# Kernel tuning notes

Hardware: AMD Instinct MI355X
Metric: run time of the kernel (lower is better)

Reference implementation:

```python
import jax, jax.numpy as jnp
import numpy as np
import math

# dims matching init_kwargs
B, N, CS, CZ = 1, 512, 384, 128
H, C, PQ, PV = 8, 128, 8, 8
INF, EPS = 1e5, 1e-8

# ---- quaternion / motor helpers (PGA motor encoded as [qw,qx,qy,qz,tx,ty,tz,0]) ----

def quat_conj(q):
    return q * jnp.array([1.0, -1.0, -1.0, -1.0], q.dtype)

def quat_mul(a, b):
    aw, ax, ay, az = jnp.split(a, 4, -1)
    bw, bx, by, bz = jnp.split(b, 4, -1)
    return jnp.concatenate([
        aw*bw - ax*bx - ay*by - az*bz,
        aw*bx + ax*bw + ay*bz - az*by,
        aw*by - ax*bz + ay*bw + az*bx,
        aw*bz + ax*by - ay*bx + az*bw], -1)

def quat_rotate(q, v):
    qv = q[..., 1:]
    uv = jnp.cross(qv, v)
    uuv = jnp.cross(qv, uv)
    return v + 2.0 * (q[..., :1] * uv + uuv)

def point_trafo(p, q, t):
    # p [...,K,3]; rigid transform by frame motor, homogeneous 4-vector out
    pp = quat_rotate(q, p) + t
    return jnp.concatenate([pp, jnp.ones_like(pp[..., :1])], -1)

def mv_transform(mv, q, t):
    # versor sandwich on a 16-dim multivector: three rotatable 3-vector blocks,
    # the point block (7:10, weight at 10) also translates; slots 0 and 10:16 invariant
    s0 = mv[..., 0:1]
    v1 = quat_rotate(q, mv[..., 1:4])
    v2 = quat_rotate(q, mv[..., 4:7])
    w = mv[..., 10:11]
    p = quat_rotate(q, mv[..., 7:10]) + w * t
    return jnp.concatenate([s0, v1, v2, p, mv[..., 10:16]], -1)

def mv_transform_inv(mv, q, t):
    qc = quat_conj(q)
    s0 = mv[..., 0:1]
    v1 = quat_rotate(qc, mv[..., 1:4])
    v2 = quat_rotate(qc, mv[..., 4:7])
    w = mv[..., 10:11]
    p = quat_rotate(qc, mv[..., 7:10] - w * t)
    return jnp.concatenate([s0, v1, v2, p, mv[..., 10:16]], -1)


def _forward(s, g, z, T, mask, W_q, b_q, W_kv, b_kv, W_qp, b_qp, W_kp, b_kp,
             W_vg, b_vg, W_mg, W_b, b_b, W_dz, b_dz, head_weights,
             softmax_weights, W_out, b_out, W_geo):
    T8 = T[..., :8]                                      # extract_motor
    qn = T8[..., :4]
    qn = qn / jnp.sqrt(jnp.sum(qn**2, -1, keepdims=True) + EPS)
    tr = T8[..., 4:7]

    q = (s @ W_q + b_q).reshape(B, N, H, C)
    kv = (s @ W_kv + b_kv).reshape(B, N, H, 2 * C)
    k, v = kv[..., :C], kv[..., C:]

    def make_pts(W, bb):
        # split into 3 chunks + stack(dim=-1) == reshape(...,3,HP).swapaxes
        p = (s @ W + bb).reshape(B, N, 3, H * PQ).swapaxes(-1, -2)  # [B,N,HP,3]
        p4 = point_trafo(p, qn[:, :, None, :], tr[:, :, None, :])
        return p4.reshape(B, N, H, PQ, 4)

    q_pts = make_pts(W_qp, b_qp)
    k_pts = make_pts(W_kp, b_kp)

    v_g = (s @ W_vg + b_vg).reshape(B, N, PV, 16)
    v_g = jnp.einsum('oi,bnic->bnoc', W_mg,
                     jnp.concatenate([v_g, g], -2)).reshape(B, N, H, PV, 16)

    bias = jnp.einsum('bijz,zh->bhij', z, W_b) + b_b[None, :, None, None]
    a = jnp.einsum('bihc,bjhc->bhij', q, k) * math.sqrt(1.0 / (3 * C))
    a = a + math.sqrt(1.0 / 3.0) * bias

    disp = q_pts[:, :, None, :, :, :3] - k_pts[:, None, :, :, :, :3]  # [B,N,N,H,P,3]
    pt = jnp.sum(disp**2, -1)                                         # [B,N,N,H,P]
    hw = jax.nn.softplus(head_weights) * math.sqrt(1.0 / (3 * (PQ * 9.0 / 2)))
    pt = -0.5 * jnp.sum(pt * hw[None, None, None, :, None], -1)       # [B,N,N,H]

    sq_mask = INF * (mask[:, :, None] * mask[:, None, :] - 1.0)
    a = a + pt.transpose(0, 3, 1, 2) + sq_mask[:, None]
    a = jax.nn.softmax(softmax_weights[None, :, None, None] * a, axis=-1)

    o = jnp.einsum('bhij,bjhc->bihc', a, v)                           # [B,N,H,C]

    qb, tb = qn[:, :, None, None, :], tr[:, :, None, None, :]
    vg_glob = mv_transform(v_g, qb, tb)
    o_g = jnp.einsum('bhij,bjhpc->bihpc', a, vg_glob)
    o_g = mv_transform_inv(o_g, qb, tb)                               # [B,N,H,PV,16]
    n1 = jnp.sqrt(jnp.sum(o_g[..., :10]**2, -1) + EPS)
    n2 = jnp.sqrt(jnp.sum(o_g[..., 10:]**2, -1) + EPS)
    o_g_norm = jnp.stack([n1, n2], -1)                                # [B,N,H,PV,2]

    # local relative frame features (8 per head)
    q_rel = quat_mul(quat_conj(qn)[:, :, None, :], qn[:, None, :, :])
    t_rel = quat_rotate(quat_conj(qn)[:, :, None, :], tr[:, None, :, :] - tr[:, :, None, :])
    rel = jnp.concatenate([q_rel, t_rel, jnp.zeros_like(t_rel[..., :1])], -1)  # [B,N,N,8]
    o_rel = jnp.einsum('bhij,bijc->bihc', a, rel)

    o_pair = jnp.einsum('bhij,bijc->bihc', a, z @ W_dz + b_dz)        # [B,N,H,CZ//4]

    feats = jnp.concatenate([o_pair, o, o_rel,
                             o_g.reshape(B, N, H, PV * 16),
                             o_g_norm.reshape(B, N, H, PV * 2)], -1).reshape(B, N, -1)
    s_out = feats @ W_out + b_out                                     # [B,N,CS]
    g_out = jnp.einsum('oi,bnic->bnoc', W_geo, o_g.reshape(B, N, H * PV, 16))
    return s_out, g_out


def setup_inputs() -> dict:
    key = jax.random.key(0)
    ks = jax.random.split(key, 32)
    def rn(i, shape, sc=1.0):
        return sc * jax.random.normal(ks[i], shape, jnp.float32)
    s = rn(0, (B, N, CS))
    g = rn(1, (B, N, PV, 16))
    z = rn(2, (B, N, N, CZ))
    Traw = rn(3, (B, N, 16))
    qn = Traw[..., :4]
    qn = qn / jnp.sqrt(jnp.sum(qn**2, -1, keepdims=True) + 1e-8)
    T = Traw.at[..., :4].set(qn).at[..., 4:7].multiply(3.0).at[..., 7:].set(0.0)
    mask = jnp.ones((B, N), jnp.float32)
    w = 0.02
    CAT = H * (CZ // 4 + C + 8 + PV * 18)   # 2496
    return dict(
        s=s, g=g, z=z, T=T, mask=mask,
        W_q=rn(4, (CS, H * C), w), b_q=jnp.zeros((H * C,), jnp.float32),
        W_kv=rn(5, (CS, 2 * H * C), w), b_kv=jnp.zeros((2 * H * C,), jnp.float32),
        W_qp=rn(6, (CS, H * PQ * 3), w), b_qp=jnp.zeros((H * PQ * 3,), jnp.float32),
        W_kp=rn(7, (CS, H * PQ * 3), w), b_kp=jnp.zeros((H * PQ * 3,), jnp.float32),
        W_vg=rn(8, (CS, PV * 16), w), b_vg=jnp.zeros((PV * 16,), jnp.float32),
        W_mg=rn(9, (H * PV, 2 * PV), 0.1),
        W_b=rn(10, (CZ, H), w), b_b=jnp.zeros((H,), jnp.float32),
        W_dz=rn(11, (CZ, CZ // 4), w), b_dz=jnp.zeros((CZ // 4,), jnp.float32),
        head_weights=-2.0 + 0.3 * rn(12, (H,)),
        softmax_weights=jnp.ones((H,), jnp.float32) + 0.1 * rn(13, (H,)),
        W_out=rn(14, (CAT, CS), w), b_out=jnp.zeros((CS,), jnp.float32),
        W_geo=rn(15, (PV, H * PV), 0.1))


def reference(s, g, z, T, mask, W_q, b_q, W_kv, b_kv, W_qp, b_qp, W_kp, b_kp,
              W_vg, b_vg, W_mg, W_b, b_b, W_dz, b_dz, head_weights,
              softmax_weights, W_out, b_out, W_geo):
    return _forward(s, g, z, T, mask, W_q, b_q, W_kv, b_kv, W_qp, b_qp, W_kp,
                    b_kp, W_vg, b_vg, W_mg, W_b, b_b, W_dz, b_dz, head_weights,
                    softmax_weights, W_out, b_out, W_geo)
```

## Files before the change

kernel.cpp:

```cpp
#include <hip/hip_runtime.h>
#include <math.h>

#define NN 512
#define CSD 384
#define CZD 128
#define HD 8
#define CD 128
#define EPSV 1e-8f
#define INFV 100000.0f

#define OFF_QN    ((size_t)0)
#define OFF_TR    ((size_t)2048)
#define OFF_QSQ   ((size_t)3584)
#define OFF_KSQ   ((size_t)7680)
#define OFF_ROWT  ((size_t)11776)
#define OFF_COLT  ((size_t)15872)
#define OFF_SB    ((size_t)19968)
#define OFF_QBUF  ((size_t)52736)
#define OFF_KV    ((size_t)577024)
#define OFF_QPTS  ((size_t)1625600)
#define OFF_KPTS  ((size_t)1723904)
#define OFF_VGG   ((size_t)1822208)
#define OFF_ZB    ((size_t)2346496)
#define OFF_A     ((size_t)4443648)
#define OFF_X     ((size_t)6540800)
#define OFF_QPR   (OFF_X)
#define OFF_KPR   (OFF_X + 98304)
#define OFF_VGR   (OFF_X + 196608)
#define OFF_U     (OFF_X)
#define OFF_V     (OFF_X + 655360)
#define OFF_AZ    (OFF_X)
#define OFF_O     (OFF_X + 524288)
#define OFF_OG    (OFF_X + 1048576)
#define OFF_FEATS (OFF_X + 1572864)
#define OFF_VP    (OFF_ZB)

__device__ __forceinline__ void qrot(const float q[4], const float* v, float* out) {
    float qw = q[0], qx = q[1], qy = q[2], qz = q[3];
    float ux = qy*v[2] - qz*v[1];
    float uy = qz*v[0] - qx*v[2];
    float uz = qx*v[1] - qy*v[0];
    float uux = qy*uz - qz*uy;
    float uuy = qz*ux - qx*uz;
    float uuz = qx*uy - qy*ux;
    out[0] = v[0] + 2.0f*(qw*ux + uux);
    out[1] = v[1] + 2.0f*(qw*uy + uuy);
    out[2] = v[2] + 2.0f*(qw*uz + uuz);
}

__device__ __forceinline__ void gemm_tiles(const float* __restrict__ A, int lda,
                                           const float* __restrict__ B, int ldb,
                                           int m0, int n0, int k0, int nk,
                                           float acc[4][4], float* AsT, float* Bs) {
    int t = threadIdx.x;
    int tx = t & 15, ty = t >> 4;
    int arow = t >> 3, ak4 = (t & 7) << 2;
    int brow = t >> 4, bc4 = (t & 15) << 2;
    const float* Ap0 = A + (size_t)(m0 + arow)*lda + ak4;
    const float* Ap1 = A + (size_t)(m0 + arow + 32)*lda + ak4;
    const float* Bp0 = B + (size_t)brow*ldb + n0 + bc4;
    const float* Bp1 = B + (size_t)(brow + 16)*ldb + n0 + bc4;
    float4 a0 = *(const float4*)(Ap0 + k0);
    float4 a1 = *(const float4*)(Ap1 + k0);
    float4 b0 = *(const float4*)(Bp0 + (size_t)k0*ldb);
    float4 b1 = *(const float4*)(Bp1 + (size_t)k0*ldb);
    for (int kc = 0; kc < nk; kc++) {
        AsT[(ak4+0)*68 + arow] = a0.x;
        AsT[(ak4+1)*68 + arow] = a0.y;
        AsT[(ak4+2)*68 + arow] = a0.z;
        AsT[(ak4+3)*68 + arow] = a0.w;
        AsT[(ak4+0)*68 + arow+32] = a1.x;
        AsT[(ak4+1)*68 + arow+32] = a1.y;
        AsT[(ak4+2)*68 + arow+32] = a1.z;
        AsT[(ak4+3)*68 + arow+32] = a1.w;
        *(float4*)(Bs + brow*64 + bc4) = b0;
        *(float4*)(Bs + (brow+16)*64 + bc4) = b1;
        __syncthreads();
        if (kc + 1 < nk) {
            int kb = k0 + (kc+1)*32;
            a0 = *(const float4*)(Ap0 + kb);
            a1 = *(const float4*)(Ap1 + kb);
            b0 = *(const float4*)(Bp0 + (size_t)kb*ldb);
            b1 = *(const float4*)(Bp1 + (size_t)kb*ldb);
        }
        #pragma unroll
        for (int kk = 0; kk < 32; kk++) {
            float4 av = *(const float4*)(AsT + kk*68 + ty*4);
            float4 bv = *(const float4*)(Bs + kk*64 + tx*4);
            acc[0][0] += av.x*bv.x; acc[0][1] += av.x*bv.y; acc[0][2] += av.x*bv.z; acc[0][3] += av.x*bv.w;
            acc[1][0] += av.y*bv.x; acc[1][1] += av.y*bv.y; acc[1][2] += av.y*bv.z; acc[1][3] += av.y*bv.w;
            acc[2][0] += av.z*bv.x; acc[2][1] += av.z*bv.y; acc[2][2] += av.z*bv.z; acc[2][3] += av.z*bv.w;
            acc[3][0] += av.w*bv.x; acc[3][1] += av.w*bv.y; acc[3][2] += av.w*bv.z; acc[3][3] += av.w*bv.w;
        }
        __syncthreads();
    }
}


__global__ void k_prep(const float* __restrict__ T, float* __restrict__ qn, float* __restrict__ tr) {
    int n = blockIdx.x*blockDim.x + threadIdx.x;
    if (n >= NN) return;
    float q0=T[n*16+0], q1=T[n*16+1], q2=T[n*16+2], q3=T[n*16+3];
    float inv = 1.0f/sqrtf(q0*q0+q1*q1+q2*q2+q3*q3 + EPSV);
    qn[n*4+0]=q0*inv; qn[n*4+1]=q1*inv; qn[n*4+2]=q2*inv; qn[n*4+3]=q3*inv;
    tr[n*3+0]=T[n*16+4]; tr[n*3+1]=T[n*16+5]; tr[n*3+2]=T[n*16+6];
}

__global__ __launch_bounds__(256) void k_proj_all(const float* __restrict__ s,
    const float* __restrict__ W_q,  const float* __restrict__ b_q,  float* __restrict__ qbuf,
    const float* __restrict__ W_kv, const float* __restrict__ b_kv, float* __restrict__ kvb,
    const float* __restrict__ W_qp, const float* __restrict__ b_qp, float* __restrict__ qpr,
    const float* __restrict__ W_kp, const float* __restrict__ b_kp, float* __restrict__ kpr,
    const float* __restrict__ W_vg, const float* __restrict__ b_vg, float* __restrict__ vgr) {
    __shared__ float AsT[32*68];
    __shared__ float Bs[32*64];
    int ny = blockIdx.y;
    const float* W; const float* bias; float* C; int N; int n0;
    if (ny < 16)      { W=W_q;  bias=b_q;  C=qbuf; N=1024; n0=ny*64; }
    else if (ny < 48) { W=W_kv; bias=b_kv; C=kvb;  N=2048; n0=(ny-16)*64; }
    else if (ny < 51) { W=W_qp; bias=b_qp; C=qpr;  N=192;  n0=(ny-48)*64; }
    else if (ny < 54) { W=W_kp; bias=b_kp; C=kpr;  N=192;  n0=(ny-51)*64; }
    else              { W=W_vg; bias=b_vg; C=vgr;  N=128;  n0=(ny-54)*64; }
    int m0 = blockIdx.x*64;
    float acc[4][4] = {};
    gemm_tiles(s, CSD, W, N, m0, n0, 0, 12, acc, AsT, Bs);
    int tx = threadIdx.x & 15, ty = threadIdx.x >> 4;
    float4 bb = *(const float4*)(bias + n0 + tx*4);
    #pragma unroll
    for (int rr = 0; rr < 4; rr++) {
        float4 o = make_float4(acc[rr][0]+bb.x, acc[rr][1]+bb.y, acc[rr][2]+bb.z, acc[rr][3]+bb.w);
        *(float4*)(C + (size_t)(m0+ty*4+rr)*N + n0 + tx*4) = o;
    }
}

__global__ __launch_bounds__(64) void k_points(const float* __restrict__ raw, const float* __restrict__ qn,
                         const float* __restrict__ tr, float* __restrict__ pts,
                         float* __restrict__ sq) {
    int n = blockIdx.x; int m = threadIdx.x;
    float p[3] = {raw[n*192 + m], raw[n*192 + 64 + m], raw[n*192 + 128 + m]};
    float q[4] = {qn[n*4],qn[n*4+1],qn[n*4+2],qn[n*4+3]};
    float r[3]; qrot(q,p,r);
    r[0]+=tr[n*3]; r[1]+=tr[n*3+1]; r[2]+=tr[n*3+2];
    pts[n*192+m*3+0]=r[0]; pts[n*192+m*3+1]=r[1]; pts[n*192+m*3+2]=r[2];
    float s = r[0]*r[0]+r[1]*r[1]+r[2]*r[2];
    s += __shfl_down(s,4,8);
    s += __shfl_down(s,2,8);
    s += __shfl_down(s,1,8);
    if ((m&7)==0) sq[n*8 + (m>>3)] = s;
}

__global__ __launch_bounds__(64) void k_vg(const float* __restrict__ vgr, const float* __restrict__ g,
                     const float* __restrict__ W_mg, const float* __restrict__ qn,
                     const float* __restrict__ tr, float* __restrict__ vgg) {
    int n = blockIdx.x; int o = threadIdx.x;
    float in[16];
    #pragma unroll
    for (int c=0;c<16;c++){
        float acc=0.0f;
        #pragma unroll
        for (int i=0;i<8;i++)  acc += W_mg[o*16+i]*vgr[n*128+i*16+c];
        #pragma unroll
        for (int i=8;i<16;i++) acc += W_mg[o*16+i]*g[n*128+(i-8)*16+c];
        in[c]=acc;
    }
    float q[4]={qn[n*4],qn[n*4+1],qn[n*4+2],qn[n*4+3]};
    float t0=tr[n*3], t1=tr[n*3+1], t2=tr[n*3+2];
    float out[16];
    out[0]=in[0];
    qrot(q,in+1,out+1);
    qrot(q,in+4,out+4);
    float w=in[10];
    qrot(q,in+7,out+7);
    out[7]+=w*t0; out[8]+=w*t1; out[9]+=w*t2;
    #pragma unroll
    for (int c=10;c<16;c++) out[c]=in[c];
    #pragma unroll
    for (int c=0;c<16;c++) vgg[(size_t)n*1024+o*16+c]=out[c];
}

__global__ __launch_bounds__(256) void k_uv(const float* __restrict__ qbuf, const float* __restrict__ kvb,
                    const float* __restrict__ qpts, const float* __restrict__ kpts,
                    const float* __restrict__ Qsq, const float* __restrict__ Ksq,
                    const float* __restrict__ hwraw, const float* __restrict__ b_b,
                    float* __restrict__ U, float* __restrict__ V,
                    float* __restrict__ rowt, float* __restrict__ colt) {
    int i = blockIdx.x; int t = threadIdx.x;
    #pragma unroll
    for (int h = 0; h < 8; h++) {
        float hw = log1pf(expf(hwraw[h])) * 0.09622504486493763f;
        if (t < 160) {
            float u, v;
            if (t < 128) {
                u = 0.05103103630798287f * qbuf[(size_t)i*1024 + h*128 + t];
                v = kvb[(size_t)i*2048 + h*256 + t];
            } else if (t < 152) {
                int d = t - 128;
                u = hw * qpts[i*192 + h*24 + d];
                v = kpts[i*192 + h*24 + d];
            } else { u = 0.0f; v = 0.0f; }
            U[((size_t)h*512 + i)*160 + t] = u;
            V[((size_t)h*160 + t)*512 + i] = v;
        }
        if (t == 160) rowt[h*512+i] = -0.5f*hw*Qsq[i*8+h] + 0.5773502691896258f*b_b[h] - INFV;
        if (t == 161) colt[h*512+i] = -0.5f*hw*Ksq[i*8+h];
    }
}

__global__ __launch_bounds__(128) void k_zb(const float* __restrict__ z,
        const float* __restrict__ W_b, float* __restrict__ zb) {
    __shared__ float zt[64*132];
    __shared__ float part[8*64];
    int i = blockIdx.x, j0 = blockIdx.y*64;
    int t = threadIdx.x;
    #pragma unroll
    for (int l = 0; l < 16; l++) {
        int f = t + l*128;
        int row = f >> 5, c4 = (f & 31) << 2;
        float4 v = *(const float4*)(z + ((size_t)(i*NN) + j0 + row)*CZD + c4);
        *(float4*)(zt + row*132 + c4) = v;
    }
    __syncthreads();
    int w = t >> 6, j = t & 63;
    int cbase = w*64;
    float acc[8] = {};
    #pragma unroll
    for (int c16 = 0; c16 < 16; c16++) {
        float4 v = *(const float4*)(zt + j*132 + cbase + c16*4);
        int c = cbase + c16*4;
        #pragma unroll
        for (int h = 0; h < 8; h++)
            acc[h] += v.x*W_b[(c+0)*8+h] + v.y*W_b[(c+1)*8+h]
                    + v.z*W_b[(c+2)*8+h] + v.w*W_b[(c+3)*8+h];
    }
    if (w == 1) {
        #pragma unroll
        for (int h = 0; h < 8; h++) part[h*64 + j] = acc[h];
    }
    __syncthreads();
    if (w == 0) {
        #pragma unroll
        for (int h = 0; h < 8; h++)
            zb[((size_t)h*512 + i)*512 + j0 + j] = acc[h] + part[h*64 + j];
    }
}

__global__ __launch_bounds__(256) void k_scorefill(const float* __restrict__ U, const float* __restrict__ V,
        const float* __restrict__ rowt, const float* __restrict__ colt,
        const float* __restrict__ zb, const float* __restrict__ mask,
        const float* __restrict__ sw, float* __restrict__ Am) {
    __shared__ float AsT[32*68];
    __shared__ float Bs[32*64];
    int h = blockIdx.z;
    int m0 = blockIdx.x*64, n0 = blockIdx.y*64;
    float acc[4][4] = {};
    gemm_tiles(U + (size_t)h*512*160, 160, V + (size_t)h*160*512, 512, m0, n0, 0, 5, acc, AsT, Bs);
    int tx = threadIdx.x & 15, ty = threadIdx.x >> 4;
    float swh = sw[h];
    float4 ct = *(const float4*)(colt + h*512 + n0 + tx*4);
    float4 mj = *(const float4*)(mask + n0 + tx*4);
    #pragma unroll
    for (int rr = 0; rr < 4; rr++) {
        int i = m0 + ty*4 + rr;
        float rt = rowt[h*512 + i];
        float mi = mask[i] * INFV;
        float4 zv = *(const float4*)(zb + ((size_t)h*512 + i)*512 + n0 + tx*4);
        float4 r;
        r.x = (acc[rr][0] + rt + ct.x + 0.5773502691896258f*zv.x + mi*mj.x)*swh;
        r.y = (acc[rr][1] + rt + ct.y + 0.5773502691896258f*zv.y + mi*mj.y)*swh;
        r.z = (acc[rr][2] + rt + ct.z + 0.5773502691896258f*zv.z + mi*mj.z)*swh;
        r.w = (acc[rr][3] + rt + ct.w + 0.5773502691896258f*zv.w + mi*mj.w)*swh;
        *(float4*)(Am + ((size_t)h*512 + i)*512 + n0 + tx*4) = r;
    }
}

__global__ __launch_bounds__(256) void k_pack(const float* __restrict__ kvb,
        const float* __restrict__ vgg, float* __restrict__ Vp) {
    int idx = blockIdx.x*256 + threadIdx.x;
    int c4 = idx & 63, j = (idx >> 6) & 511, h = idx >> 15;
    int col = c4*4;
    float4 v;
    if (col < 128) v = *(const float4*)(kvb + (size_t)j*2048 + h*256 + 128 + col);
    else           v = *(const float4*)(vgg + (size_t)j*1024 + h*128 + col - 128);
    *(float4*)(Vp + ((size_t)h*512 + j)*256 + col) = v;
}

__global__ __launch_bounds__(256) void k_softmax(float* __restrict__ Am,
        const float* __restrict__ qn, const float* __restrict__ tr, float* __restrict__ S) {
    __shared__ float red[8];
    __shared__ float sred[4][8];
    int row = blockIdx.x;
    float* p = Am + (size_t)row*512;
    int t = threadIdx.x;
    float x0 = p[t], x1 = p[t+256];
    float m = fmaxf(x0, x1);
    #pragma unroll
    for (int o = 32; o > 0; o >>= 1) m = fmaxf(m, __shfl_xor(m, o));
    int wv = t >> 6, ln = t & 63;
    if (ln == 0) red[wv] = m;
    __syncthreads();
    m = fmaxf(fmaxf(red[0], red[1]), fmaxf(red[2], red[3]));
    float e0 = expf(x0 - m), e1 = expf(x1 - m);
    float sm = e0 + e1;
    #pragma unroll
    for (int o = 32; o > 0; o >>= 1) sm += __shfl_xor(sm, o);
    __syncthreads();
    if (ln == 0) red[4 + wv] = sm;
    __syncthreads();
    float inv = 1.0f / (red[4]+red[5]+red[6]+red[7]);
    float a0 = e0*inv, a1 = e1*inv;
    p[t] = a0;
    p[t+256] = a1;
    float4 q0 = *(const float4*)(qn + t*4);
    float4 q1 = *(const float4*)(qn + (t+256)*4);
    float acc[8];
    acc[0] = a0*q0.x + a1*q1.x;
    acc[1] = a0*q0.y + a1*q1.y;
    acc[2] = a0*q0.z + a1*q1.z;
    acc[3] = a0*q0.w + a1*q1.w;
    acc[4] = a0*tr[t*3+0] + a1*tr[(t+256)*3+0];
    acc[5] = a0*tr[t*3+1] + a1*tr[(t+256)*3+1];
    acc[6] = a0*tr[t*3+2] + a1*tr[(t+256)*3+2];
    acc[7] = a0 + a1;
    #pragma unroll
    for (int c = 0; c < 8; c++) {
        #pragma unroll
        for (int o = 32; o > 0; o >>= 1) acc[c] += __shfl_xor(acc[c], o);
    }
    if (ln == 0) {
        #pragma unroll
        for (int c = 0; c < 8; c++) sred[wv][c] = acc[c];
    }
    __syncthreads();
    if (t < 8) {
        int h = row >> 9, i = row & 511;
        S[i*64 + h*8 + t] = sred[0][t]+sred[1][t]+sred[2][t]+sred[3][t];
    }
}

__global__ __launch_bounds__(256) void k_apply(const float* __restrict__ Am,
        const float* __restrict__ Vp, float* __restrict__ obuf, float* __restrict__ og) {
    __shared__ float AsT[32*68];
    __shared__ float Bs[32*64];
    int m0 = blockIdx.x*64;
    int n0 = blockIdx.y*64;
    int h = blockIdx.z & 7, js = blockIdx.z >> 3;
    float acc[4][4] = {};
    gemm_tiles(Am + (size_t)h*512*512, 512, Vp + (size_t)h*512*256, 256,
               m0, n0, js*256, 8, acc, AsT, Bs);
    int tx = threadIdx.x & 15, ty = threadIdx.x >> 4;
    float* base = (n0 < 128) ? (obuf + h*128 + n0) : (og + h*128 + n0 - 128);
    #pragma unroll
    for (int rr = 0; rr < 4; rr++) {
        #pragma unroll
        for (int cc = 0; cc < 4; cc++)
            atomicAdd(base + (size_t)(m0+ty*4+rr)*1024 + tx*4 + cc, acc[rr][cc]);
    }
}

__global__ __launch_bounds__(256) void k_az(const float* __restrict__ Am,
        const float* __restrict__ z, float* __restrict__ az) {
    __shared__ float aT[512*8];
    __shared__ float part[3*1024];
    int i = blockIdx.x, t = threadIdx.x;
    #pragma unroll
    for (int l = 0; l < 16; l++) {
        int f = t + l*256;
        int h = f >> 9, j = f & 511;
        aT[j*8 + h] = Am[((size_t)h*512 + i)*512 + j];
    }
    __syncthreads();
    int c2 = t & 63, quarter = t >> 6;
    int jb = quarter*128;
    float acc[8][2] = {};
    for (int j = jb; j < jb+128; j++) {
        float2 zv = *(const float2*)(z + ((size_t)(i*NN) + j)*CZD + c2*2);
        float4 a0 = *(const float4*)(aT + j*8);
        float4 a1 = *(const float4*)(aT + j*8 + 4);
        acc[0][0] += a0.x*zv.x; acc[0][1] += a0.x*zv.y;
        acc[1][0] += a0.y*zv.x; acc[1][1] += a0.y*zv.y;
        acc[2][0] += a0.z*zv.x; acc[2][1] += a0.z*zv.y;
        acc[3][0] += a0.w*zv.x; acc[3][1] += a0.w*zv.y;
        acc[4][0] += a1.x*zv.x; acc[4][1] += a1.x*zv.y;
        acc[5][0] += a1.y*zv.x; acc[5][1] += a1.y*zv.y;
        acc[6][0] += a1.z*zv.x; acc[6][1] += a1.z*zv.y;
        acc[7][0] += a1.w*zv.x; acc[7][1] += a1.w*zv.y;
    }
    if (quarter > 0) {
        #pragma unroll
        for (int h = 0; h < 8; h++) {
            part[(quarter-1)*1024 + h*128 + c2*2 + 0] = acc[h][0];
            part[(quarter-1)*1024 + h*128 + c2*2 + 1] = acc[h][1];
        }
    }
    __syncthreads();
    if (quarter == 0) {
        #pragma unroll
        for (int h = 0; h < 8; h++) {
            #pragma unroll
            for (int d = 0; d < 2; d++) {
                float sum = acc[h][d] + part[h*128 + c2*2 + d]
                          + part[1024 + h*128 + c2*2 + d] + part[2048 + h*128 + c2*2 + d];
                az[(size_t)i*1024 + h*128 + c2*2 + d] = sum;
            }
        }
    }
}

__global__ __launch_bounds__(128) void k_finalize(const float* __restrict__ obuf, const float* __restrict__ az,
                           const float* __restrict__ W_dz, const float* __restrict__ b_dz,
                           float* __restrict__ og, const float* __restrict__ S,
                           const float* __restrict__ qn, const float* __restrict__ tr,
                           float* __restrict__ feats) {
    int i=blockIdx.x, h=blockIdx.y, t=threadIdx.x;
    float* f = feats + (size_t)i*2496 + h*312;
    f[32+t] = obuf[(size_t)i*1024+h*128+t];
    if (t < 32) {
        float acc = b_dz[t];
        const float* azr = az + (size_t)i*1024 + h*128;
        #pragma unroll 4
        for (int zc=0;zc<128;zc++) acc += azr[zc]*W_dz[zc*32+t];
        f[t]=acc;
    } else if (t >= 64 && t < 72) {
        int p = t-64;
        float* ogp = og + (size_t)i*1024 + h*128 + p*16;
        float in[16];
        #pragma unroll
        for (int c=0;c<16;c++) in[c]=ogp[c];
        float qc[4]={qn[i*4], -qn[i*4+1], -qn[i*4+2], -qn[i*4+3]};
        float t0=tr[i*3], t1=tr[i*3+1], t2=tr[i*3+2];
        float out[16];
        out[0]=in[0];
        qrot(qc,in+1,out+1);
        qrot(qc,in+4,out+4);
        float w=in[10];
        float tmp[3]={in[7]-w*t0, in[8]-w*t1, in[9]-w*t2};
        qrot(qc,tmp,out+7);
        #pragma unroll
        for (int c2=10;c2<16;c2++) out[c2]=in[c2];
        float n1=EPSV, n2=EPSV;
        #pragma unroll
        for (int c2=0;c2<10;c2++) n1 += out[c2]*out[c2];
        #pragma unroll
        for (int c2=10;c2<16;c2++) n2 += out[c2]*out[c2];
        n1=sqrtf(n1); n2=sqrtf(n2);
        #pragma unroll
        for (int c2=0;c2<16;c2++){ f[168+p*16+c2]=out[c2]; ogp[c2]=out[c2]; }
        f[296+p*2]=n1; f[296+p*2+1]=n2;
    } else if (t == 96) {
        float qc0=qn[i*4], qc1=-qn[i*4+1], qc2=-qn[i*4+2], qc3=-qn[i*4+3];
        const float* Sr = S + i*64 + h*8;
        float b0=Sr[0], b1=Sr[1], b2=Sr[2], b3=Sr[3];
        f[160] = qc0*b0 - qc1*b1 - qc2*b2 - qc3*b3;
        f[161] = qc0*b1 + qc1*b0 + qc2*b3 - qc3*b2;
        f[162] = qc0*b2 - qc1*b3 + qc2*b0 + qc3*b1;
        f[163] = qc0*b3 + qc1*b2 - qc2*b1 + qc3*b0;
        float A = Sr[7];
        float v[3]={Sr[4]-A*tr[i*3], Sr[5]-A*tr[i*3+1], Sr[6]-A*tr[i*3+2]};
        float qc[4]={qc0,qc1,qc2,qc3};
        float r[3]; qrot(qc,v,r);
        f[164]=r[0]; f[165]=r[1]; f[166]=r[2]; f[167]=0.0f;
    }
}

__global__ __launch_bounds__(256) void k_gout(const float* __restrict__ og, const float* __restrict__ W_geo,
                       float* __restrict__ gout) {
    int idx = blockIdx.x*blockDim.x+threadIdx.x;
    int c = idx & 15;
    int o = (idx>>4) & 7;
    int n = idx >> 7;
    float acc=0.0f;
    #pragma unroll 4
    for (int i2=0;i2<64;i2++) acc += W_geo[o*64+i2]*og[(size_t)n*1024 + i2*16 + c];
    gout[(size_t)n*128 + o*16 + c]=acc;
}

__global__ __launch_bounds__(256) void k_sout(const float* __restrict__ feats,
        const float* __restrict__ W_out, const float* __restrict__ b_out, float* __restrict__ out) {
    __shared__ float AsT[32*68];
    __shared__ float Bs[32*64];
    int m0 = blockIdx.x*64, n0 = blockIdx.y*64, kz = blockIdx.z;
    float acc[4][4] = {};
    gemm_tiles(feats, 2496, W_out, CSD, m0, n0, kz*416, 13, acc, AsT, Bs);
    int tx = threadIdx.x & 15, ty = threadIdx.x >> 4;
    #pragma unroll
    for (int rr = 0; rr < 4; rr++) {
        #pragma unroll
        for (int cc = 0; cc < 4; cc++) {
            float v = acc[rr][cc];
            if (kz == 0) v += b_out[n0 + tx*4 + cc];
            atomicAdd(out + (size_t)(m0+ty*4+rr)*CSD + n0 + tx*4 + cc, v);
        }
    }
}


extern "C" void kernel_launch(void* const* d_in, const int* in_sizes, int n_in,
                              void* d_out, int out_size, void* d_ws, size_t ws_size,
                              hipStream_t stream) {
    const float* s     = (const float*)d_in[0];
    const float* g     = (const float*)d_in[1];
    const float* z     = (const float*)d_in[2];
    const float* T     = (const float*)d_in[3];
    const float* mask  = (const float*)d_in[4];
    const float* W_q   = (const float*)d_in[5];
    const float* b_q   = (const float*)d_in[6];
    const float* W_kv  = (const float*)d_in[7];
    const float* b_kv  = (const float*)d_in[8];
    const float* W_qp  = (const float*)d_in[9];
    const float* b_qp  = (const float*)d_in[10];
    const float* W_kp  = (const float*)d_in[11];
    const float* b_kp  = (const float*)d_in[12];
    const float* W_vg  = (const float*)d_in[13];
    const float* b_vg  = (const float*)d_in[14];
    const float* W_mg  = (const float*)d_in[15];
    const float* W_b   = (const float*)d_in[16];
    const float* b_b   = (const float*)d_in[17];
    const float* W_dz  = (const float*)d_in[18];
    const float* b_dz  = (const float*)d_in[19];
    const float* hw    = (const float*)d_in[20];
    const float* sw    = (const float*)d_in[21];
    const float* W_out = (const float*)d_in[22];
    const float* b_out = (const float*)d_in[23];
    const float* W_geo = (const float*)d_in[24];

    float* ws   = (float*)d_ws;
    float* out  = (float*)d_out;

    float* qn   = ws + OFF_QN;
    float* tr   = ws + OFF_TR;
    float* Qsq  = ws + OFF_QSQ;
    float* Ksq  = ws + OFF_KSQ;
    float* rowt = ws + OFF_ROWT;
    float* colt = ws + OFF_COLT;
    float* Sbuf = ws + OFF_SB;
    float* qbuf = ws + OFF_QBUF;
    float* kvb  = ws + OFF_KV;
    float* qpts = ws + OFF_QPTS;
    float* kpts = ws + OFF_KPTS;
    float* vgg  = ws + OFF_VGG;
    float* zb   = ws + OFF_ZB;
    float* Am   = ws + OFF_A;
    float* qpr  = ws + OFF_QPR;
    float* kpr  = ws + OFF_KPR;
    float* vgr  = ws + OFF_VGR;
    float* U    = ws + OFF_U;
    float* V    = ws + OFF_V;
    float* az   = ws + OFF_AZ;
    float* obuf = ws + OFF_O;
    float* og   = ws + OFF_OG;
    float* feats= ws + OFF_FEATS;
    float* Vp   = ws + OFF_VP;

    hipMemsetAsync(out, 0, (size_t)NN*CSD*sizeof(float), stream);

    k_prep<<<2,256,0,stream>>>(T,qn,tr);
    k_proj_all<<<dim3(8,56),256,0,stream>>>(s, W_q,b_q,qbuf, W_kv,b_kv,kvb,
                                            W_qp,b_qp,qpr, W_kp,b_kp,kpr, W_vg,b_vg,vgr);
    k_points<<<NN,64,0,stream>>>(qpr,qn,tr,qpts,Qsq);
    k_points<<<NN,64,0,stream>>>(kpr,qn,tr,kpts,Ksq);
    k_vg<<<NN,64,0,stream>>>(vgr,g,W_mg,qn,tr,vgg);
    k_uv<<<NN,256,0,stream>>>(qbuf,kvb,qpts,kpts,Qsq,Ksq,hw,b_b,U,V,rowt,colt);
    k_zb<<<dim3(NN,8),128,0,stream>>>(z,W_b,zb);
    k_scorefill<<<dim3(8,8,8),256,0,stream>>>(U,V,rowt,colt,zb,mask,sw,Am);
    k_pack<<<1024,256,0,stream>>>(kvb,vgg,Vp);
    hipMemsetAsync(ws + OFF_O, 0, (size_t)2*512*1024*sizeof(float), stream);
    k_softmax<<<4096,256,0,stream>>>(Am,qn,tr,Sbuf);
    k_apply<<<dim3(8,4,16),256,0,stream>>>(Am,Vp,obuf,og);
    k_az<<<NN,256,0,stream>>>(Am,z,az);
    k_finalize<<<dim3(NN,HD),128,0,stream>>>(obuf,az,W_dz,b_dz,og,Sbuf,qn,tr,feats);
    k_gout<<<256,256,0,stream>>>(og,W_geo,out + (size_t)NN*CSD);
    k_sout<<<dim3(8,6,6),256,0,stream>>>(feats,W_out,b_out,out);
}
```

Before: 464.1 us.

## Fuse geometry prep kernels and replace atomic split-K with slab reductions

Merges prep, point transforms, value-geometry, UV building and V packing into one per-residue kernel that keeps points in shared memory. It also fuses az, finalize and geo output into one kernel. The split-K atomics in apply and the output projection become plain stores into separate slabs that are summed afterwards, which removes two memsets. The aim is fewer launches and fewer global round-trips and atomics, at the cost of more workspace and an extra reduction pass.

```diff
diff --git a/kernel.cpp b/kernel.cpp
--- a/kernel.cpp
+++ b/kernel.cpp
@@ -11,29 +11,25 @@
 
 #define OFF_QN    ((size_t)0)
 #define OFF_TR    ((size_t)2048)
-#define OFF_QSQ   ((size_t)3584)
-#define OFF_KSQ   ((size_t)7680)
-#define OFF_ROWT  ((size_t)11776)
-#define OFF_COLT  ((size_t)15872)
-#define OFF_SB    ((size_t)19968)
-#define OFF_QBUF  ((size_t)52736)
-#define OFF_KV    ((size_t)577024)
-#define OFF_QPTS  ((size_t)1625600)
-#define OFF_KPTS  ((size_t)1723904)
-#define OFF_VGG   ((size_t)1822208)
-#define OFF_ZB    ((size_t)2346496)
-#define OFF_A     ((size_t)4443648)
-#define OFF_X     ((size_t)6540800)
-#define OFF_QPR   (OFF_X)
-#define OFF_KPR   (OFF_X + 98304)
-#define OFF_VGR   (OFF_X + 196608)
-#define OFF_U     (OFF_X)
-#define OFF_V     (OFF_X + 655360)
-#define OFF_AZ    (OFF_X)
-#define OFF_O     (OFF_X + 524288)
-#define OFF_OG    (OFF_X + 1048576)
-#define OFF_FEATS (OFF_X + 1572864)
-#define OFF_VP    (OFF_ZB)
+#define OFF_ROWT  ((size_t)4096)
+#define OFF_COLT  ((size_t)8192)
+#define OFF_SB    ((size_t)12288)
+#define OFF_QBUF  ((size_t)45056)
+#define OFF_KV    ((size_t)569344)
+#define OFF_QPR   ((size_t)1617920)
+#define OFF_KPR   ((size_t)1716224)
+#define OFF_VGR   ((size_t)1814528)
+#define OFF_ZB    ((size_t)1880064)
+#define OFF_A     ((size_t)3977216)
+#define OFF_U     ((size_t)6074368)
+#define OFF_V     ((size_t)6729728)
+#define OFF_VP    ((size_t)7385088)
+#define OFF_OB0   ((size_t)8433664)
+#define OFF_OB1   ((size_t)8957952)
+#define OFF_OG0   ((size_t)9482240)
+#define OFF_OG1   ((size_t)10006528)
+#define OFF_FEATS ((size_t)10530816)
+#define OFF_PS    ((size_t)11808768)
 
 __device__ __forceinline__ void qrot(const float q[4], const float* v, float* out) {
     float qw = q[0], qx = q[1], qy = q[2], qz = q[3];
@@ -97,15 +93,6 @@
 }
 
 
-__global__ void k_prep(const float* __restrict__ T, float* __restrict__ qn, float* __restrict__ tr) {
-    int n = blockIdx.x*blockDim.x + threadIdx.x;
-    if (n >= NN) return;
-    float q0=T[n*16+0], q1=T[n*16+1], q2=T[n*16+2], q3=T[n*16+3];
-    float inv = 1.0f/sqrtf(q0*q0+q1*q1+q2*q2+q3*q3 + EPSV);
-    qn[n*4+0]=q0*inv; qn[n*4+1]=q1*inv; qn[n*4+2]=q2*inv; qn[n*4+3]=q3*inv;
-    tr[n*3+0]=T[n*16+4]; tr[n*3+1]=T[n*16+5]; tr[n*3+2]=T[n*16+6];
-}
-
 __global__ __launch_bounds__(256) void k_proj_all(const float* __restrict__ s,
     const float* __restrict__ W_q,  const float* __restrict__ b_q,  float* __restrict__ qbuf,
     const float* __restrict__ W_kv, const float* __restrict__ b_kv, float* __restrict__ kvb,
@@ -133,76 +120,99 @@
     }
 }
 
-__global__ __launch_bounds__(64) void k_points(const float* __restrict__ raw, const float* __restrict__ qn,
-                         const float* __restrict__ tr, float* __restrict__ pts,
-                         float* __restrict__ sq) {
-    int n = blockIdx.x; int m = threadIdx.x;
-    float p[3] = {raw[n*192 + m], raw[n*192 + 64 + m], raw[n*192 + 128 + m]};
-    float q[4] = {qn[n*4],qn[n*4+1],qn[n*4+2],qn[n*4+3]};
-    float r[3]; qrot(q,p,r);
-    r[0]+=tr[n*3]; r[1]+=tr[n*3+1]; r[2]+=tr[n*3+2];
-    pts[n*192+m*3+0]=r[0]; pts[n*192+m*3+1]=r[1]; pts[n*192+m*3+2]=r[2];
-    float s = r[0]*r[0]+r[1]*r[1]+r[2]*r[2];
-    s += __shfl_down(s,4,8);
-    s += __shfl_down(s,2,8);
-    s += __shfl_down(s,1,8);
-    if ((m&7)==0) sq[n*8 + (m>>3)] = s;
-}
-
-__global__ __launch_bounds__(64) void k_vg(const float* __restrict__ vgr, const float* __restrict__ g,
-                     const float* __restrict__ W_mg, const float* __restrict__ qn,
-                     const float* __restrict__ tr, float* __restrict__ vgg) {
-    int n = blockIdx.x; int o = threadIdx.x;
-    float in[16];
-    #pragma unroll
-    for (int c=0;c<16;c++){
-        float acc=0.0f;
-        #pragma unroll
-        for (int i=0;i<8;i++)  acc += W_mg[o*16+i]*vgr[n*128+i*16+c];
-        #pragma unroll
-        for (int i=8;i<16;i++) acc += W_mg[o*16+i]*g[n*128+(i-8)*16+c];
-        in[c]=acc;
-    }
-    float q[4]={qn[n*4],qn[n*4+1],qn[n*4+2],qn[n*4+3]};
-    float t0=tr[n*3], t1=tr[n*3+1], t2=tr[n*3+2];
-    float out[16];
-    out[0]=in[0];
-    qrot(q,in+1,out+1);
-    qrot(q,in+4,out+4);
-    float w=in[10];
-    qrot(q,in+7,out+7);
-    out[7]+=w*t0; out[8]+=w*t1; out[9]+=w*t2;
-    #pragma unroll
-    for (int c=10;c<16;c++) out[c]=in[c];
-    #pragma unroll
-    for (int c=0;c<16;c++) vgg[(size_t)n*1024+o*16+c]=out[c];
-}
-
-__global__ __launch_bounds__(256) void k_uv(const float* __restrict__ qbuf, const float* __restrict__ kvb,
-                    const float* __restrict__ qpts, const float* __restrict__ kpts,
-                    const float* __restrict__ Qsq, const float* __restrict__ Ksq,
-                    const float* __restrict__ hwraw, const float* __restrict__ b_b,
-                    float* __restrict__ U, float* __restrict__ V,
-                    float* __restrict__ rowt, float* __restrict__ colt) {
-    int i = blockIdx.x; int t = threadIdx.x;
+__global__ __launch_bounds__(256) void k_geo(
+    const float* __restrict__ T,
+    const float* __restrict__ qpr, const float* __restrict__ kpr,
+    const float* __restrict__ vgr, const float* __restrict__ g,
+    const float* __restrict__ W_mg,
+    const float* __restrict__ qbuf, const float* __restrict__ kvb,
+    const float* __restrict__ hwraw, const float* __restrict__ b_b,
+    float* __restrict__ qn, float* __restrict__ tr,
+    float* __restrict__ U, float* __restrict__ V,
+    float* __restrict__ rowt, float* __restrict__ colt,
+    float* __restrict__ Vp)
+{
+    __shared__ float s_q[4];
+    __shared__ float s_t[3];
+    __shared__ float s_qpts[192], s_kpts[192];
+    __shared__ float s_Qsq[8], s_Ksq[8];
+    int n = blockIdx.x, t = threadIdx.x;
+    if (t == 0) {
+        float q0=T[n*16+0], q1=T[n*16+1], q2=T[n*16+2], q3=T[n*16+3];
+        float inv = 1.0f/sqrtf(q0*q0+q1*q1+q2*q2+q3*q3 + EPSV);
+        float a0=q0*inv, a1=q1*inv, a2=q2*inv, a3=q3*inv;
+        s_q[0]=a0; s_q[1]=a1; s_q[2]=a2; s_q[3]=a3;
+        float u0=T[n*16+4], u1=T[n*16+5], u2=T[n*16+6];
+        s_t[0]=u0; s_t[1]=u1; s_t[2]=u2;
+        qn[n*4+0]=a0; qn[n*4+1]=a1; qn[n*4+2]=a2; qn[n*4+3]=a3;
+        tr[n*3+0]=u0; tr[n*3+1]=u1; tr[n*3+2]=u2;
+    }
+    __syncthreads();
+    float q[4]={s_q[0],s_q[1],s_q[2],s_q[3]};
+    float t0=s_t[0], t1=s_t[1], t2=s_t[2];
+    if (t < 128) {
+        int m = t & 63;
+        const float* raw = (t < 64) ? qpr : kpr;
+        float p[3] = {raw[n*192 + m], raw[n*192 + 64 + m], raw[n*192 + 128 + m]};
+        float r[3]; qrot(q,p,r);
+        r[0]+=t0; r[1]+=t1; r[2]+=t2;
+        float* dp = (t<64) ? s_qpts : s_kpts;
+        dp[m*3+0]=r[0]; dp[m*3+1]=r[1]; dp[m*3+2]=r[2];
+        float ss = r[0]*r[0]+r[1]*r[1]+r[2]*r[2];
+        ss += __shfl_down(ss,4,8);
+        ss += __shfl_down(ss,2,8);
+        ss += __shfl_down(ss,1,8);
+        if ((m&7)==0) ((t<64)?s_Qsq:s_Ksq)[m>>3] = ss;
+    } else if (t < 192) {
+        int o = t - 128;
+        float in[16];
+        #pragma unroll
+        for (int c=0;c<16;c++){
+            float acc=0.0f;
+            #pragma unroll
+            for (int i=0;i<8;i++)  acc += W_mg[o*16+i]*vgr[n*128+i*16+c];
+            #pragma unroll
+            for (int i=8;i<16;i++) acc += W_mg[o*16+i]*g[n*128+(i-8)*16+c];
+            in[c]=acc;
+        }
+        float out[16];
+        out[0]=in[0];
+        qrot(q,in+1,out+1);
+        qrot(q,in+4,out+4);
+        float w=in[10];
+        qrot(q,in+7,out+7);
+        out[7]+=w*t0; out[8]+=w*t1; out[9]+=w*t2;
+        #pragma unroll
+        for (int c=10;c<16;c++) out[c]=in[c];
+        int h=o>>3, pp=o&7;
+        float* vp = Vp + ((size_t)(h*512+n))*256 + 128 + pp*16;
+        #pragma unroll
+        for (int c=0;c<16;c++) vp[c]=out[c];
+    }
+    #pragma unroll
+    for (int l=0;l<4;l++){
+        int f = t + l*256; int h = f>>7, c = f&127;
+        Vp[((size_t)(h*512+n))*256 + c] = kvb[(size_t)n*2048 + h*256 + 128 + c];
+    }
+    __syncthreads();
     #pragma unroll
     for (int h = 0; h < 8; h++) {
-        float hw = log1pf(expf(hwraw[h])) * 0.09622504486493763f;
+        float hwv = log1pf(expf(hwraw[h])) * 0.09622504486493763f;
         if (t < 160) {
             float u, v;
             if (t < 128) {
-                u = 0.05103103630798287f * qbuf[(size_t)i*1024 + h*128 + t];
-                v = kvb[(size_t)i*2048 + h*256 + t];
+                u = 0.05103103630798287f * qbuf[(size_t)n*1024 + h*128 + t];
+                v = kvb[(size_t)n*2048 + h*256 + t];
             } else if (t < 152) {
                 int d = t - 128;
-                u = hw * qpts[i*192 + h*24 + d];
-                v = kpts[i*192 + h*24 + d];
+                u = hwv * s_qpts[h*24 + d];
+                v = s_kpts[h*24 + d];
             } else { u = 0.0f; v = 0.0f; }
-            U[((size_t)h*512 + i)*160 + t] = u;
-            V[((size_t)h*160 + t)*512 + i] = v;
+            U[((size_t)h*512 + n)*160 + t] = u;
+            V[((size_t)h*160 + t)*512 + n] = v;
         }
-        if (t == 160) rowt[h*512+i] = -0.5f*hw*Qsq[i*8+h] + 0.5773502691896258f*b_b[h] - INFV;
-        if (t == 161) colt[h*512+i] = -0.5f*hw*Ksq[i*8+h];
+        if (t == 160) rowt[h*512+n] = -0.5f*hwv*s_Qsq[h] + 0.5773502691896258f*b_b[h] - INFV;
+        if (t == 161) colt[h*512+n] = -0.5f*hwv*s_Ksq[h];
     }
 }
 
@@ -271,17 +281,6 @@
         r.w = (acc[rr][3] + rt + ct.w + 0.5773502691896258f*zv.w + mi*mj.w)*swh;
         *(float4*)(Am + ((size_t)h*512 + i)*512 + n0 + tx*4) = r;
     }
-}
-
-__global__ __launch_bounds__(256) void k_pack(const float* __restrict__ kvb,
-        const float* __restrict__ vgg, float* __restrict__ Vp) {
-    int idx = blockIdx.x*256 + threadIdx.x;
-    int c4 = idx & 63, j = (idx >> 6) & 511, h = idx >> 15;
-    int col = c4*4;
-    float4 v;
-    if (col < 128) v = *(const float4*)(kvb + (size_t)j*2048 + h*256 + 128 + col);
-    else           v = *(const float4*)(vgg + (size_t)j*1024 + h*128 + col - 128);
-    *(float4*)(Vp + ((size_t)h*512 + j)*256 + col) = v;
 }
 
 __global__ __launch_bounds__(256) void k_softmax(float* __restrict__ Am,
@@ -338,7 +337,8 @@
 }
 
 __global__ __launch_bounds__(256) void k_apply(const float* __restrict__ Am,
-        const float* __restrict__ Vp, float* __restrict__ obuf, float* __restrict__ og) {
+        const float* __restrict__ Vp, float* __restrict__ ob0, float* __restrict__ ob1,
+        float* __restrict__ og0, float* __restrict__ og1) {
     __shared__ float AsT[32*68];
     __shared__ float Bs[32*64];
     int m0 = blockIdx.x*64;
@@ -348,19 +348,29 @@
     gemm_tiles(Am + (size_t)h*512*512, 512, Vp + (size_t)h*512*256, 256,
                m0, n0, js*256, 8, acc, AsT, Bs);
     int tx = threadIdx.x & 15, ty = threadIdx.x >> 4;
+    float* obuf = js ? ob1 : ob0;
+    float* og   = js ? og1 : og0;
     float* base = (n0 < 128) ? (obuf + h*128 + n0) : (og + h*128 + n0 - 128);
     #pragma unroll
     for (int rr = 0; rr < 4; rr++) {
-        #pragma unroll
-        for (int cc = 0; cc < 4; cc++)
-            atomicAdd(base + (size_t)(m0+ty*4+rr)*1024 + tx*4 + cc, acc[rr][cc]);
-    }
-}
-
-__global__ __launch_bounds__(256) void k_az(const float* __restrict__ Am,
-        const float* __restrict__ z, float* __restrict__ az) {
+        *(float4*)(base + (size_t)(m0+ty*4+rr)*1024 + tx*4) =
+            make_float4(acc[rr][0], acc[rr][1], acc[rr][2], acc[rr][3]);
+    }
+}
+
+__global__ __launch_bounds__(256) void k_azfin(
+    const float* __restrict__ Am, const float* __restrict__ z,
+    const float* __restrict__ ob0, const float* __restrict__ ob1,
+    const float* __restrict__ og0, const float* __restrict__ og1,
+    const float* __restrict__ W_dz, const float* __restrict__ b_dz,
+    const float* __restrict__ S, const float* __restrict__ qn, const float* __restrict__ tr,
+    const float* __restrict__ W_geo,
+    float* __restrict__ feats, float* __restrict__ outg)
+{
     __shared__ float aT[512*8];
     __shared__ float part[3*1024];
+    __shared__ float s_az[1024];
+    __shared__ float s_og[1024];
     int i = blockIdx.x, t = threadIdx.x;
     #pragma unroll
     for (int l = 0; l < 16; l++) {
@@ -398,36 +408,35 @@
         for (int h = 0; h < 8; h++) {
             #pragma unroll
             for (int d = 0; d < 2; d++) {
-                float sum = acc[h][d] + part[h*128 + c2*2 + d]
+                s_az[h*128 + c2*2 + d] = acc[h][d] + part[h*128 + c2*2 + d]
                           + part[1024 + h*128 + c2*2 + d] + part[2048 + h*128 + c2*2 + d];
-                az[(size_t)i*1024 + h*128 + c2*2 + d] = sum;
             }
         }
     }
-}
-
-__global__ __launch_bounds__(128) void k_finalize(const float* __restrict__ obuf, const float* __restrict__ az,
-                           const float* __restrict__ W_dz, const float* __restrict__ b_dz,
-                           float* __restrict__ og, const float* __restrict__ S,
-                           const float* __restrict__ qn, const float* __restrict__ tr,
-                           float* __restrict__ feats) {
-    int i=blockIdx.x, h=blockIdx.y, t=threadIdx.x;
-    float* f = feats + (size_t)i*2496 + h*312;
-    f[32+t] = obuf[(size_t)i*1024+h*128+t];
-    if (t < 32) {
-        float acc = b_dz[t];
-        const float* azr = az + (size_t)i*1024 + h*128;
+    __syncthreads();
+    float* f = feats + (size_t)i*2496;
+    #pragma unroll
+    for (int l = 0; l < 4; l++) {
+        int ff = t + l*256; int h = ff>>7, c = ff&127;
+        f[h*312 + 32 + c] = ob0[(size_t)i*1024 + h*128 + c] + ob1[(size_t)i*1024 + h*128 + c];
+    }
+    {
+        int h = t >> 5, cdz = t & 31;
+        float a2 = b_dz[cdz];
         #pragma unroll 4
-        for (int zc=0;zc<128;zc++) acc += azr[zc]*W_dz[zc*32+t];
-        f[t]=acc;
-    } else if (t >= 64 && t < 72) {
-        int p = t-64;
-        float* ogp = og + (size_t)i*1024 + h*128 + p*16;
+        for (int zc = 0; zc < 128; zc++) a2 += s_az[h*128 + zc]*W_dz[zc*32 + cdz];
+        f[h*312 + cdz] = a2;
+    }
+    float qc0=qn[i*4], qc1=-qn[i*4+1], qc2=-qn[i*4+2], qc3=-qn[i*4+3];
+    float t0=tr[i*3], t1=tr[i*3+1], t2=tr[i*3+2];
+    if (t < 64) {
+        int h = t >> 3, p = t & 7;
+        const float* a0 = og0 + (size_t)i*1024 + h*128 + p*16;
+        const float* a1 = og1 + (size_t)i*1024 + h*128 + p*16;
         float in[16];
         #pragma unroll
-        for (int c=0;c<16;c++) in[c]=ogp[c];
-        float qc[4]={qn[i*4], -qn[i*4+1], -qn[i*4+2], -qn[i*4+3]};
-        float t0=tr[i*3], t1=tr[i*3+1], t2=tr[i*3+2];
+        for (int c=0;c<16;c++) in[c]=a0[c]+a1[c];
+        float qc[4]={qc0,qc1,qc2,qc3};
         float out[16];
         out[0]=in[0];
         qrot(qc,in+1,out+1);
@@ -436,61 +445,66 @@
         float tmp[3]={in[7]-w*t0, in[8]-w*t1, in[9]-w*t2};
         qrot(qc,tmp,out+7);
         #pragma unroll
-        for (int c2=10;c2<16;c2++) out[c2]=in[c2];
+        for (int c2x=10;c2x<16;c2x++) out[c2x]=in[c2x];
         float n1=EPSV, n2=EPSV;
         #pragma unroll
-        for (int c2=0;c2<10;c2++) n1 += out[c2]*out[c2];
-        #pragma unroll
-        for (int c2=10;c2<16;c2++) n2 += out[c2]*out[c2];
+        for (int c2x=0;c2x<10;c2x++) n1 += out[c2x]*out[c2x];
+        #pragma unroll
+        for (int c2x=10;c2x<16;c2x++) n2 += out[c2x]*out[c2x];
         n1=sqrtf(n1); n2=sqrtf(n2);
         #pragma unroll
-        for (int c2=0;c2<16;c2++){ f[168+p*16+c2]=out[c2]; ogp[c2]=out[c2]; }
-        f[296+p*2]=n1; f[296+p*2+1]=n2;
-    } else if (t == 96) {
-        float qc0=qn[i*4], qc1=-qn[i*4+1], qc2=-qn[i*4+2], qc3=-qn[i*4+3];
+        for (int c2x=0;c2x<16;c2x++){ f[h*312+168+p*16+c2x]=out[c2x]; s_og[t*16+c2x]=out[c2x]; }
+        f[h*312+296+p*2]=n1; f[h*312+296+p*2+1]=n2;
+    } else if (t < 72) {
+        int h = t - 64;
         const float* Sr = S + i*64 + h*8;
         float b0=Sr[0], b1=Sr[1], b2=Sr[2], b3=Sr[3];
-        f[160] = qc0*b0 - qc1*b1 - qc2*b2 - qc3*b3;
-        f[161] = qc0*b1 + qc1*b0 + qc2*b3 - qc3*b2;
-        f[162] = qc0*b2 - qc1*b3 + qc2*b0 + qc3*b1;
-        f[163] = qc0*b3 + qc1*b2 - qc2*b1 + qc3*b0;
+        f[h*312+160] = qc0*b0 - qc1*b1 - qc2*b2 - qc3*b3;
+        f[h*312+161] = qc0*b1 + qc1*b0 + qc2*b3 - qc3*b2;
+        f[h*312+162] = qc0*b2 - qc1*b3 + qc2*b0 + qc3*b1;
+        f[h*312+163] = qc0*b3 + qc1*b2 - qc2*b1 + qc3*b0;
         float A = Sr[7];
-        float v[3]={Sr[4]-A*tr[i*3], Sr[5]-A*tr[i*3+1], Sr[6]-A*tr[i*3+2]};
+        float v[3]={Sr[4]-A*t0, Sr[5]-A*t1, Sr[6]-A*t2};
         float qc[4]={qc0,qc1,qc2,qc3};
         float r[3]; qrot(qc,v,r);
-        f[164]=r[0]; f[165]=r[1]; f[166]=r[2]; f[167]=0.0f;
-    }
-}
-
-__global__ __launch_bounds__(256) void k_gout(const float* __restrict__ og, const float* __restrict__ W_geo,
-                       float* __restrict__ gout) {
-    int idx = blockIdx.x*blockDim.x+threadIdx.x;
-    int c = idx & 15;
-    int o = (idx>>4) & 7;
-    int n = idx >> 7;
-    float acc=0.0f;
-    #pragma unroll 4
-    for (int i2=0;i2<64;i2++) acc += W_geo[o*64+i2]*og[(size_t)n*1024 + i2*16 + c];
-    gout[(size_t)n*128 + o*16 + c]=acc;
+        f[h*312+164]=r[0]; f[h*312+165]=r[1]; f[h*312+166]=r[2]; f[h*312+167]=0.0f;
+    }
+    __syncthreads();
+    if (t < 128) {
+        int o = (t>>4) & 7, c = t & 15;
+        float a3 = 0.0f;
+        #pragma unroll 4
+        for (int i2=0;i2<64;i2++) a3 += W_geo[o*64+i2]*s_og[i2*16+c];
+        outg[(size_t)i*128 + o*16 + c] = a3;
+    }
 }
 
 __global__ __launch_bounds__(256) void k_sout(const float* __restrict__ feats,
-        const float* __restrict__ W_out, const float* __restrict__ b_out, float* __restrict__ out) {
+        const float* __restrict__ W_out, float* __restrict__ Ps) {
     __shared__ float AsT[32*68];
     __shared__ float Bs[32*64];
     int m0 = blockIdx.x*64, n0 = blockIdx.y*64, kz = blockIdx.z;
     float acc[4][4] = {};
     gemm_tiles(feats, 2496, W_out, CSD, m0, n0, kz*416, 13, acc, AsT, Bs);
     int tx = threadIdx.x & 15, ty = threadIdx.x >> 4;
+    float* slab = Ps + (size_t)kz*512*384;
     #pragma unroll
     for (int rr = 0; rr < 4; rr++) {
-        #pragma unroll
-        for (int cc = 0; cc < 4; cc++) {
-            float v = acc[rr][cc];
-            if (kz == 0) v += b_out[n0 + tx*4 + cc];
-            atomicAdd(out + (size_t)(m0+ty*4+rr)*CSD + n0 + tx*4 + cc, v);
-        }
-    }
+        *(float4*)(slab + (size_t)(m0+ty*4+rr)*CSD + n0 + tx*4) =
+            make_float4(acc[rr][0], acc[rr][1], acc[rr][2], acc[rr][3]);
+    }
+}
+
+__global__ __launch_bounds__(256) void k_sout_red(const float* __restrict__ Ps,
+        const float* __restrict__ b_out, float* __restrict__ out) {
+    int idx = (blockIdx.x*256 + threadIdx.x)*4;
+    float4 s = *(const float4*)(b_out + (idx % 384));
+    #pragma unroll
+    for (int kz = 0; kz < 6; kz++) {
+        float4 p = *(const float4*)(Ps + (size_t)kz*196608 + idx);
+        s.x += p.x; s.y += p.y; s.z += p.z; s.w += p.w;
+    }
+    *(float4*)(out + idx) = s;
 }
 
 
@@ -528,46 +542,36 @@
 
     float* qn   = ws + OFF_QN;
     float* tr   = ws + OFF_TR;
-    float* Qsq  = ws + OFF_QSQ;
-    float* Ksq  = ws + OFF_KSQ;
     float* rowt = ws + OFF_ROWT;
     float* colt = ws + OFF_COLT;
     float* Sbuf = ws + OFF_SB;
     float* qbuf = ws + OFF_QBUF;
     float* kvb  = ws + OFF_KV;
-    float* qpts = ws + OFF_QPTS;
-    float* kpts = ws + OFF_KPTS;
-    float* vgg  = ws + OFF_VGG;
-    float* zb   = ws + OFF_ZB;
-    float* Am   = ws + OFF_A;
     float* qpr  = ws + OFF_QPR;
     float* kpr  = ws + OFF_KPR;
     float* vgr  = ws + OFF_VGR;
+    float* zb   = ws + OFF_ZB;
+    float* Am   = ws + OFF_A;
     float* U    = ws + OFF_U;
     float* V    = ws + OFF_V;
-    float* az   = ws + OFF_AZ;
-    float* obuf = ws + OFF_O;
-    float* og   = ws + OFF_OG;
+    float* Vp   = ws + OFF_VP;
+    float* ob0  = ws + OFF_OB0;
+    float* ob1  = ws + OFF_OB1;
+    float* og0  = ws + OFF_OG0;
+    float* og1  = ws + OFF_OG1;
     float* feats= ws + OFF_FEATS;
-    float* Vp   = ws + OFF_VP;
-
-    hipMemsetAsync(out, 0, (size_t)NN*CSD*sizeof(float), stream);
-
-    k_prep<<<2,256,0,stream>>>(T,qn,tr);
+    float* Ps   = ws + OFF_PS;
+
     k_proj_all<<<dim3(8,56),256,0,stream>>>(s, W_q,b_q,qbuf, W_kv,b_kv,kvb,
                                             W_qp,b_qp,qpr, W_kp,b_kp,kpr, W_vg,b_vg,vgr);
-    k_points<<<NN,64,0,stream>>>(qpr,qn,tr,qpts,Qsq);
-    k_points<<<NN,64,0,stream>>>(kpr,qn,tr,kpts,Ksq);
-    k_vg<<<NN,64,0,stream>>>(vgr,g,W_mg,qn,tr,vgg);
-    k_uv<<<NN,256,0,stream>>>(qbuf,kvb,qpts,kpts,Qsq,Ksq,hw,b_b,U,V,rowt,colt);
+    k_geo<<<NN,256,0,stream>>>(T,qpr,kpr,vgr,g,W_mg,qbuf,kvb,hw,b_b,
+                               qn,tr,U,V,rowt,colt,Vp);
     k_zb<<<dim3(NN,8),128,0,stream>>>(z,W_b,zb);
     k_scorefill<<<dim3(8,8,8),256,0,stream>>>(U,V,rowt,colt,zb,mask,sw,Am);
-    k_pack<<<1024,256,0,stream>>>(kvb,vgg,Vp);
-    hipMemsetAsync(ws + OFF_O, 0, (size_t)2*512*1024*sizeof(float), stream);
     k_softmax<<<4096,256,0,stream>>>(Am,qn,tr,Sbuf);
-    k_apply<<<dim3(8,4,16),256,0,stream>>>(Am,Vp,obuf,og);
-    k_az<<<NN,256,0,stream>>>(Am,z,az);
-    k_finalize<<<dim3(NN,HD),128,0,stream>>>(obuf,az,W_dz,b_dz,og,Sbuf,qn,tr,feats);
-    k_gout<<<256,256,0,stream>>>(og,W_geo,out + (size_t)NN*CSD);
-    k_sout<<<dim3(8,6,6),256,0,stream>>>(feats,W_out,b_out,out);
-}
+    k_apply<<<dim3(8,4,16),256,0,stream>>>(Am,Vp,ob0,ob1,og0,og1);
+    k_azfin<<<NN,256,0,stream>>>(Am,z,ob0,ob1,og0,og1,W_dz,b_dz,Sbuf,qn,tr,W_geo,
+                                 feats, out + (size_t)NN*CSD);
+    k_sout<<<dim3(8,6,6),256,0,stream>>>(feats,W_out,Ps);
+    k_sout_red<<<192,256,0,stream>>>(Ps,b_out,out);
+}
```

Result: faster. 405.1 us (-12.7%).
